# Kernel optimization log

Measured on AMD Instinct MI355X. Metric: run time of the kernel, lower is better.

Reference implementation:

```python
import jax, jax.numpy as jnp
import numpy as np

K_TOP = 2  # top-k experts per token


def setup_inputs() -> dict:
    key = jax.random.key(0)
    k1, k2, k3 = jax.random.split(key, 3)
    B, S, H, E = 4, 2048, 1024, 8
    hidden_states = jax.random.normal(k1, (B, S, H), dtype=jnp.float32)
    router_w = jax.random.normal(k2, (E, H), dtype=jnp.float32) * 0.02
    expert_weights = jax.random.normal(k3, (E, H, H), dtype=jnp.float32) * 0.02
    return {"hidden_states": hidden_states, "router_w": router_w, "expert_weights": expert_weights}


def reference(hidden_states, router_w, expert_weights):
    B, S, H = hidden_states.shape
    x = hidden_states.reshape(-1, H)                      # [N, H], N = B*S
    logits = x @ router_w.T                               # [N, E]
    probs = jax.nn.softmax(logits, axis=-1)               # [N, E]
    topk_vals, topk_idx = jax.lax.top_k(probs, K_TOP)     # [N, K]
    topk_w = topk_vals / (topk_vals.sum(-1, keepdims=True) + 1e-6)  # [N, K]

    # Dense per-expert GEMM over all tokens (single-device dispatch = identity)
    expert_out = jnp.einsum('nh,eho->eno', x, expert_weights)  # [E, N, H]

    # all_to_all_combine: gather each token's K expert outputs
    combined = jnp.take_along_axis(
        expert_out.transpose(1, 0, 2),                    # [N, E, H]
        topk_idx[:, :, None], axis=1)                     # [N, K, H]
    combined = combined.transpose(1, 0, 2)                # [K, N, H]

    # remap bias: sum over last dim of one-hot(topk_idx) * router_prob == gathered prob
    remap_bias = jnp.take_along_axis(probs, topk_idx, axis=1).T[:, :, None]  # [K, N, 1]

    weights = topk_w.T[:, :, None]                        # [K, N, 1]
    out = ((combined + remap_bias) * weights).sum(axis=0) # [N, H]
    return out.reshape(B, S, H)
```

## Files before the change

kernel.cpp:

```cpp
#include <hip/hip_runtime.h>
#include <hip/hip_fp16.h>
#include <cstdint>

typedef unsigned short u16;
typedef __attribute__((ext_vector_type(8))) short short8;
typedef __attribute__((ext_vector_type(4))) float float4v;

#define NTOK 8192
#define HDIM 1024
#define NEXP 8
#define TM 128
#define TN 128
#define BK 32
#define NITER (HDIM / BK)
#define ABUF (TM * BK)
#define MAXT 136
#define WBLK 8192
#define RBLK 2048

__device__ __forceinline__ u16 f2bf(float f) {
    union { float f; uint32_t u; } v; v.f = f;
    uint32_t u = v.u;
    return (u16)((u + 0x7FFFu + ((u >> 16) & 1u)) >> 16);
}

__device__ __forceinline__ void gll16(const u16* g, u16* l) {
    __builtin_amdgcn_global_load_lds(
        (const __attribute__((address_space(1))) uint32_t*)g,
        (__attribute__((address_space(3))) uint32_t*)l,
        16, 0, 0);
}

__global__ __launch_bounds__(256) void prep(const float* __restrict__ x,
                                            const float* __restrict__ rw,
                                            const float* __restrict__ ew,
                                            u16* __restrict__ x_bf,
                                            u16* __restrict__ w_bf,
                                            float* __restrict__ wt0,
                                            float* __restrict__ wt1,
                                            float* __restrict__ biasv,
                                            int* __restrict__ sel,
                                            int* __restrict__ ctrl) {
    if (blockIdx.x == 0 && threadIdx.x < 132) ctrl[threadIdx.x] = 0;

    if (blockIdx.x < WBLK) {
        __shared__ float tile[32][33];
        const int bid = blockIdx.x;
        const int e  = bid >> 10;
        const int k0 = (bid & 31) * 32;
        const int n0 = ((bid >> 5) & 31) * 32;
        const int r = threadIdx.x >> 3;
        const int c = (threadIdx.x & 7) * 4;
        const float4 v = *(const float4*)(ew + ((size_t)e << 20) + (size_t)(k0 + r) * HDIM + n0 + c);
        tile[r][c] = v.x; tile[r][c+1] = v.y; tile[r][c+2] = v.z; tile[r][c+3] = v.w;
        __syncthreads();
        ushort4 o;
        o.x = f2bf(tile[c][r]); o.y = f2bf(tile[c+1][r]);
        o.z = f2bf(tile[c+2][r]); o.w = f2bf(tile[c+3][r]);
        *(ushort4*)(w_bf + ((size_t)e << 20) + (size_t)(n0 + r) * HDIM + k0 + c) = o;
    } else {
        const int wv = threadIdx.x >> 6;
        const int l  = threadIdx.x & 63;
        const int n  = (blockIdx.x - WBLK) * 4 + wv;
        const float4* xr = (const float4*)(x + (size_t)n * HDIM);
        ushort4* xo = (ushort4*)(x_bf + (size_t)n * HDIM);

        float4 xv[4];
#pragma unroll
        for (int t = 0; t < 4; t++) {
            xv[t] = xr[t * 64 + l];
            ushort4 p;
            p.x = f2bf(xv[t].x); p.y = f2bf(xv[t].y);
            p.z = f2bf(xv[t].z); p.w = f2bf(xv[t].w);
            xo[t * 64 + l] = p;
        }

        float logits[NEXP];
#pragma unroll
        for (int e = 0; e < NEXP; e++) {
            const float4* rwe = (const float4*)(rw + e * HDIM);
            float acc = 0.f;
#pragma unroll
            for (int t = 0; t < 4; t++) {
                const float4 r = rwe[t * 64 + l];
                acc += xv[t].x * r.x + xv[t].y * r.y + xv[t].z * r.z + xv[t].w * r.w;
            }
#pragma unroll
            for (int s = 32; s > 0; s >>= 1) acc += __shfl_xor(acc, s, 64);
            logits[e] = acc;
        }

        if (l == 0) {
            float mx = logits[0];
#pragma unroll
            for (int e = 1; e < NEXP; e++) mx = fmaxf(mx, logits[e]);
            float p[NEXP]; float sum = 0.f;
#pragma unroll
            for (int e = 0; e < NEXP; e++) { p[e] = expf(logits[e] - mx); sum += p[e]; }
            const float inv = 1.f / sum;
#pragma unroll
            for (int e = 0; e < NEXP; e++) p[e] *= inv;
            int e0 = 0;
#pragma unroll
            for (int e = 1; e < NEXP; e++) if (p[e] > p[e0]) e0 = e;
            int e1 = (e0 == 0) ? 1 : 0;
#pragma unroll
            for (int e = 0; e < NEXP; e++) if (e != e0 && p[e] > p[e1]) e1 = e;
            const float p0 = p[e0], p1 = p[e1];
            const float wsum = p0 + p1 + 1e-6f;
            const float w0 = p0 / wsum, w1 = p1 / wsum;
            wt0[n] = w0; wt1[n] = w1;
            biasv[n] = w0 * p0 + w1 * p1;
            sel[n] = e0 | (e1 << 8);
        }
    }
}

__global__ __launch_bounds__(256) void build_lists(const int* __restrict__ sel,
                                                   int* __restrict__ lists,
                                                   int* __restrict__ ctrl,
                                                   int* __restrict__ tmap) {
    const int n  = blockIdx.x * 256 + threadIdx.x;
    const int wv = threadIdx.x >> 6;
    const int l  = threadIdx.x & 63;
    const int s  = sel[n];
    const int e0 = s & 0xFF, e1 = s >> 8;
    __shared__ int wcnt[NEXP][4];
    __shared__ int ebase[NEXP];
    int pf0 = 0, pf1 = 0;
    const unsigned long long ltmask = (1ULL << l) - 1ULL;
#pragma unroll
    for (int e = 0; e < NEXP; e++) {
        const int slot = (e0 == e) ? 0 : ((e1 == e) ? 1 : -1);
        const unsigned long long bal = __ballot(slot >= 0);
        const int pf = __popcll(bal & ltmask);
        if (slot == 0) pf0 = pf;
        if (slot == 1) pf1 = pf;
        if (l == 0) wcnt[e][wv] = __popcll(bal);
    }
    __syncthreads();
    if (threadIdx.x < NEXP) {
        const int e = threadIdx.x;
        const int tot = wcnt[e][0] + wcnt[e][1] + wcnt[e][2] + wcnt[e][3];
        ebase[e] = atomicAdd(&ctrl[e * 16], tot);
    }
    __syncthreads();
    int off0 = ebase[e0], off1 = ebase[e1];
#pragma unroll
    for (int i = 0; i < 4; i++) {
        off0 += (i < wv) ? wcnt[e0][i] : 0;
        off1 += (i < wv) ? wcnt[e1][i] : 0;
    }
    lists[e0 * NTOK + off0 + pf0] = n;
    lists[e1 * NTOK + off1 + pf1] = n | 0x10000;

    __shared__ int lastflag;
    __threadfence();
    if (threadIdx.x == 0) lastflag = (atomicAdd(&ctrl[128], 1) == (int)gridDim.x - 1);
    __syncthreads();
    if (lastflag) {
        __shared__ int tbase[NEXP + 1];
        if (threadIdx.x == 0) {
            int acc = 0;
            for (int e = 0; e < NEXP; e++) {
                tbase[e] = acc;
                acc += (atomicAdd(&ctrl[e * 16], 0) + TM - 1) / TM;
            }
            tbase[NEXP] = acc;
        }
        __syncthreads();
        for (int i = threadIdx.x; i < MAXT; i += 256) {
            int v = -1;
#pragma unroll
            for (int e = 0; e < NEXP; e++)
                if (i >= tbase[e] && i < tbase[e + 1]) v = (e << 16) | (i - tbase[e]);
            tmap[i] = v;
        }
    }
}

__global__ __launch_bounds__(256) void moe_gemm(const u16* __restrict__ x_bf,
                                                const u16* __restrict__ wt_bf,
                                                const int* __restrict__ lists,
                                                const int* __restrict__ ctrl,
                                                const int* __restrict__ tmap,
                                                const float* __restrict__ wt0,
                                                const float* __restrict__ wt1,
                                                const float* __restrict__ biasv,
                                                __half* __restrict__ stage0,
                                                __half* __restrict__ stage1) {
    const int ent = tmap[blockIdx.x];
    if (ent < 0) return;
    const int e = ent >> 16;
    const int tile_m = (ent & 0xFFFF) * TM;
    const int cnt = ctrl[e * 16];
    const int tn = blockIdx.y * TN;

    __shared__ u16 lA[3 * ABUF];
    __shared__ u16 lB[3 * ABUF];
    __shared__ int   toks[TM];
    __shared__ float wgt[TM];
    __shared__ float bia[TM];
    __shared__ int   slt[TM];

    const int t  = threadIdx.x;
    const int wv = t >> 6;
    const int l  = t & 63;

    if (t < TM) {
        const int idx = tile_m + t;
        int tok = 0; float w = 0.f, b = 0.f; int sl = 0;
        if (idx < cnt) {
            const int entry = lists[e * NTOK + idx];
            tok = entry & 0xFFFF;
            sl = entry >> 16;
            w = sl ? wt1[tok] : wt0[tok];
            b = sl ? 0.f : biasv[tok];
        }
        toks[t] = tok; wgt[t] = w; bia[t] = b; slt[t] = sl;
    }
    __syncthreads();

    const int r_in = l >> 2;
    const int koff = ((l & 3) ^ (r_in & 3)) * 8;
    const u16* pA[2]; const u16* pB[2]; int qoff[2];
#pragma unroll
    for (int i = 0; i < 2; i++) {
        const int c = wv * 2 + i;
        const int row = c * 16 + r_in;
        pA[i] = x_bf + (size_t)toks[row] * HDIM + koff;
        pB[i] = wt_bf + ((size_t)e << 20) + (size_t)(tn + row) * HDIM + koff;
        qoff[i] = c * 512;
    }

    const int wm = (wv & 1) * 64;
    const int wn = (wv >> 1) * 64;
    const int fm = l & 15;
    const int fq = l >> 4;
    int aoff[4], boff[4];
#pragma unroll
    for (int i = 0; i < 4; i++) {
        const int ra = wm + i * 16 + fm;
        const int rb = wn + i * 16 + fm;
        aoff[i] = ra * 32 + ((fq ^ (ra & 3)) * 8);
        boff[i] = rb * 32 + ((fq ^ (rb & 3)) * 8);
    }

    float4v acc[4][4];
#pragma unroll
    for (int i = 0; i < 4; i++)
#pragma unroll
        for (int j = 0; j < 4; j++) { float4v z = {0.f, 0.f, 0.f, 0.f}; acc[i][j] = z; }

    gll16(pA[0], lA + qoff[0]);
    gll16(pA[1], lA + qoff[1]);
    gll16(pB[0], lB + qoff[0]);
    gll16(pB[1], lB + qoff[1]);

    int cur = 0, nxt = 1;
    for (int it = 0; it < NITER; ++it) {
        if (it < NITER - 1) {
            const int nk = (it + 1) * BK;
            u16* la = lA + nxt * ABUF;
            u16* lb = lB + nxt * ABUF;
            gll16(pA[0] + nk, la + qoff[0]);
            gll16(pA[1] + nk, la + qoff[1]);
            gll16(pB[0] + nk, lb + qoff[0]);
            gll16(pB[1] + nk, lb + qoff[1]);
            asm volatile("s_waitcnt vmcnt(4)\n\ts_barrier" ::: "memory");
        } else {
            asm volatile("s_waitcnt vmcnt(0)\n\ts_barrier" ::: "memory");
        }

        const u16* ca = lA + cur * ABUF;
        const u16* cb = lB + cur * ABUF;
        short8 af[4], bf[4];
#pragma unroll
        for (int mf = 0; mf < 4; mf++) af[mf] = *(const short8*)&ca[aoff[mf]];
#pragma unroll
        for (int nf = 0; nf < 4; nf++) bf[nf] = *(const short8*)&cb[boff[nf]];
#pragma unroll
        for (int mf = 0; mf < 4; mf++)
#pragma unroll
            for (int nf = 0; nf < 4; nf++)
                acc[mf][nf] = __builtin_amdgcn_mfma_f32_16x16x32_bf16(af[mf], bf[nf], acc[mf][nf], 0, 0, 0);

        cur = nxt;
        nxt = (nxt == 2) ? 0 : nxt + 1;
    }

#pragma unroll
    for (int mf = 0; mf < 4; mf++) {
#pragma unroll
        for (int r = 0; r < 4; r++) {
            const int m_local = wm + mf * 16 + fq * 4 + r;
            if (tile_m + m_local < cnt) {
                const int tok = toks[m_local];
                const float w = wgt[m_local], b = bia[m_local];
                __half* sp = (slt[m_local] ? stage1 : stage0) + (size_t)tok * HDIM;
#pragma unroll
                for (int nf = 0; nf < 4; nf++) {
                    const int h = tn + wn + nf * 16 + fm;
                    sp[h] = __float2half(acc[mf][nf][r] * w + b);
                }
            }
        }
    }
}

__global__ __launch_bounds__(256) void combine(const __half* __restrict__ s0,
                                               const __half* __restrict__ s1,
                                               float* __restrict__ out) {
    const size_t idx = ((size_t)blockIdx.x * 256 + threadIdx.x) * 8;
    union { uint4 v; __half h[8]; } a, b;
    a.v = *(const uint4*)(s0 + idx);
    b.v = *(const uint4*)(s1 + idx);
    float4 o0, o1;
    o0.x = __half2float(a.h[0]) + __half2float(b.h[0]);
    o0.y = __half2float(a.h[1]) + __half2float(b.h[1]);
    o0.z = __half2float(a.h[2]) + __half2float(b.h[2]);
    o0.w = __half2float(a.h[3]) + __half2float(b.h[3]);
    o1.x = __half2float(a.h[4]) + __half2float(b.h[4]);
    o1.y = __half2float(a.h[5]) + __half2float(b.h[5]);
    o1.z = __half2float(a.h[6]) + __half2float(b.h[6]);
    o1.w = __half2float(a.h[7]) + __half2float(b.h[7]);
    *(float4*)(out + idx)     = o0;
    *(float4*)(out + idx + 4) = o1;
}

extern "C" void kernel_launch(void* const* d_in, const int* in_sizes, int n_in,
                              void* d_out, int out_size, void* d_ws, size_t ws_size,
                              hipStream_t stream) {
    const float* x  = (const float*)d_in[0];
    const float* rw = (const float*)d_in[1];
    const float* ew = (const float*)d_in[2];
    float* out = (float*)d_out;

    char* ws = (char*)d_ws;
    u16*    x_bf   = (u16*)ws;
    u16*    w_bf   = (u16*)(ws + 16777216);
    __half* stage0 = (__half*)(ws + 33554432);
    __half* stage1 = (__half*)(ws + 50331648);
    float*  wt0    = (float*)(ws + 67108864);
    float*  wt1    = (float*)(ws + 67141632);
    float*  biasv  = (float*)(ws + 67174400);
    int*    sel    = (int*)(ws + 67207168);
    int*    lists  = (int*)(ws + 67239936);
    int*    ctrl   = (int*)(ws + 67502080);
    int*    tmap   = (int*)(ws + 67502720);

    prep<<<WBLK + RBLK, 256, 0, stream>>>(x, rw, ew, x_bf, w_bf, wt0, wt1, biasv, sel, ctrl);
    build_lists<<<NTOK / 256, 256, 0, stream>>>(sel, lists, ctrl, tmap);
    moe_gemm<<<dim3(MAXT, HDIM / TN, 1), 256, 0, stream>>>(
        x_bf, w_bf, lists, ctrl, tmap, wt0, wt1, biasv, stage0, stage1);
    combine<<<(NTOK * HDIM) / (256 * 8), 256, 0, stream>>>(stage0, stage1, out);
}
```

Before: 201.9 us.

## Widen MoE GEMM tile to 128x256 with double-buffered LDS and new swizzle

Doubles the N tile so each block computes 128x256, with each wave owning a 64-column strip across all 128 rows (8x4 MFMA fragments per wave). This raises operand reuse per byte loaded from global memory. The LDS pipeline drops from triple to double buffering with a full wait at the top of each iteration, and the swizzle changes to XOR on (row>>1)&3. It also adds s_setprio around the MFMA bursts and caps occupancy at 2 blocks. In exchange it doubles the accumulator registers, halves the grid size in N, and may expose load latency because prefetch now overlaps less with compute.

```diff
diff --git a/kernel.cpp b/kernel.cpp
--- a/kernel.cpp
+++ b/kernel.cpp
@@ -10,10 +10,11 @@
 #define HDIM 1024
 #define NEXP 8
 #define TM 128
-#define TN 128
+#define TN 256
 #define BK 32
 #define NITER (HDIM / BK)
-#define ABUF (TM * BK)
+#define LA_N (TM * BK)
+#define LB_N (TN * BK)
 #define MAXT 136
 #define WBLK 8192
 #define RBLK 2048
@@ -179,16 +180,16 @@
     }
 }
 
-__global__ __launch_bounds__(256) void moe_gemm(const u16* __restrict__ x_bf,
-                                                const u16* __restrict__ wt_bf,
-                                                const int* __restrict__ lists,
-                                                const int* __restrict__ ctrl,
-                                                const int* __restrict__ tmap,
-                                                const float* __restrict__ wt0,
-                                                const float* __restrict__ wt1,
-                                                const float* __restrict__ biasv,
-                                                __half* __restrict__ stage0,
-                                                __half* __restrict__ stage1) {
+__global__ __launch_bounds__(256, 2) void moe_gemm(const u16* __restrict__ x_bf,
+                                                   const u16* __restrict__ wt_bf,
+                                                   const int* __restrict__ lists,
+                                                   const int* __restrict__ ctrl,
+                                                   const int* __restrict__ tmap,
+                                                   const float* __restrict__ wt0,
+                                                   const float* __restrict__ wt1,
+                                                   const float* __restrict__ biasv,
+                                                   __half* __restrict__ stage0,
+                                                   __half* __restrict__ stage1) {
     const int ent = tmap[blockIdx.x];
     if (ent < 0) return;
     const int e = ent >> 16;
@@ -196,8 +197,8 @@
     const int cnt = ctrl[e * 16];
     const int tn = blockIdx.y * TN;
 
-    __shared__ u16 lA[3 * ABUF];
-    __shared__ u16 lB[3 * ABUF];
+    __shared__ u16 lA[2 * LA_N];
+    __shared__ u16 lB[2 * LB_N];
     __shared__ int   toks[TM];
     __shared__ float wgt[TM];
     __shared__ float bia[TM];
@@ -221,86 +222,94 @@
     }
     __syncthreads();
 
-    const int r_in = l >> 2;
-    const int koff = ((l & 3) ^ (r_in & 3)) * 8;
-    const u16* pA[2]; const u16* pB[2]; int qoff[2];
+    const u16* gA[2]; int dA[2];
 #pragma unroll
     for (int i = 0; i < 2; i++) {
-        const int c = wv * 2 + i;
-        const int row = c * 16 + r_in;
-        pA[i] = x_bf + (size_t)toks[row] * HDIM + koff;
-        pB[i] = wt_bf + ((size_t)e << 20) + (size_t)(tn + row) * HDIM + koff;
-        qoff[i] = c * 512;
-    }
-
-    const int wm = (wv & 1) * 64;
-    const int wn = (wv >> 1) * 64;
+        const int slot = (i * 4 + wv) * 64 + l;
+        const int row  = slot >> 2;
+        const int c    = (slot & 3) ^ ((row >> 1) & 3);
+        gA[i] = x_bf + (size_t)toks[row] * HDIM + c * 8;
+        dA[i] = (i * 4 + wv) * 512;
+    }
+    const u16* gB[4]; int dB[4];
+#pragma unroll
+    for (int i = 0; i < 4; i++) {
+        const int slot = (i * 4 + wv) * 64 + l;
+        const int row  = slot >> 2;
+        const int c    = (slot & 3) ^ ((row >> 1) & 3);
+        gB[i] = wt_bf + ((size_t)e << 20) + (size_t)(tn + row) * HDIM + c * 8;
+        dB[i] = (i * 4 + wv) * 512;
+    }
+
     const int fm = l & 15;
     const int fq = l >> 4;
-    int aoff[4], boff[4];
-#pragma unroll
-    for (int i = 0; i < 4; i++) {
-        const int ra = wm + i * 16 + fm;
-        const int rb = wn + i * 16 + fm;
-        aoff[i] = ra * 32 + ((fq ^ (ra & 3)) * 8);
-        boff[i] = rb * 32 + ((fq ^ (rb & 3)) * 8);
-    }
-
-    float4v acc[4][4];
-#pragma unroll
-    for (int i = 0; i < 4; i++)
+    int aoff[8], boff[4];
+#pragma unroll
+    for (int mf = 0; mf < 8; mf++) {
+        const int r = mf * 16 + fm;
+        aoff[mf] = r * BK + ((fq ^ ((r >> 1) & 3)) * 8);
+    }
+#pragma unroll
+    for (int nf = 0; nf < 4; nf++) {
+        const int r = wv * 64 + nf * 16 + fm;
+        boff[nf] = r * BK + ((fq ^ ((r >> 1) & 3)) * 8);
+    }
+
+    float4v acc[8][4];
+#pragma unroll
+    for (int i = 0; i < 8; i++)
 #pragma unroll
         for (int j = 0; j < 4; j++) { float4v z = {0.f, 0.f, 0.f, 0.f}; acc[i][j] = z; }
 
-    gll16(pA[0], lA + qoff[0]);
-    gll16(pA[1], lA + qoff[1]);
-    gll16(pB[0], lB + qoff[0]);
-    gll16(pB[1], lB + qoff[1]);
-
-    int cur = 0, nxt = 1;
+#pragma unroll
+    for (int i = 0; i < 2; i++) gll16(gA[i], lA + dA[i]);
+#pragma unroll
+    for (int i = 0; i < 4; i++) gll16(gB[i], lB + dB[i]);
+
     for (int it = 0; it < NITER; ++it) {
-        if (it < NITER - 1) {
+        asm volatile("s_waitcnt vmcnt(0) lgkmcnt(0)\n\ts_barrier" ::: "memory");
+        if (it + 1 < NITER) {
             const int nk = (it + 1) * BK;
-            u16* la = lA + nxt * ABUF;
-            u16* lb = lB + nxt * ABUF;
-            gll16(pA[0] + nk, la + qoff[0]);
-            gll16(pA[1] + nk, la + qoff[1]);
-            gll16(pB[0] + nk, lb + qoff[0]);
-            gll16(pB[1] + nk, lb + qoff[1]);
-            asm volatile("s_waitcnt vmcnt(4)\n\ts_barrier" ::: "memory");
-        } else {
-            asm volatile("s_waitcnt vmcnt(0)\n\ts_barrier" ::: "memory");
-        }
-
-        const u16* ca = lA + cur * ABUF;
-        const u16* cb = lB + cur * ABUF;
-        short8 af[4], bf[4];
-#pragma unroll
-        for (int mf = 0; mf < 4; mf++) af[mf] = *(const short8*)&ca[aoff[mf]];
-#pragma unroll
-        for (int nf = 0; nf < 4; nf++) bf[nf] = *(const short8*)&cb[boff[nf]];
-#pragma unroll
-        for (int mf = 0; mf < 4; mf++)
-#pragma unroll
-            for (int nf = 0; nf < 4; nf++)
-                acc[mf][nf] = __builtin_amdgcn_mfma_f32_16x16x32_bf16(af[mf], bf[nf], acc[mf][nf], 0, 0, 0);
-
-        cur = nxt;
-        nxt = (nxt == 2) ? 0 : nxt + 1;
-    }
-
-#pragma unroll
-    for (int mf = 0; mf < 4; mf++) {
+            u16* la = lA + ((it + 1) & 1) * LA_N;
+            u16* lb = lB + ((it + 1) & 1) * LB_N;
+#pragma unroll
+            for (int i = 0; i < 2; i++) gll16(gA[i] + nk, la + dA[i]);
+#pragma unroll
+            for (int i = 0; i < 4; i++) gll16(gB[i] + nk, lb + dB[i]);
+        }
+        const u16* ca = lA + (it & 1) * LA_N;
+        const u16* cb = lB + (it & 1) * LB_N;
+        short8 bfr[4];
+#pragma unroll
+        for (int nf = 0; nf < 4; nf++) bfr[nf] = *(const short8*)&cb[boff[nf]];
+#pragma unroll
+        for (int mh = 0; mh < 2; mh++) {
+            short8 afr[4];
+#pragma unroll
+            for (int i = 0; i < 4; i++) afr[i] = *(const short8*)&ca[aoff[mh * 4 + i]];
+            __builtin_amdgcn_s_setprio(1);
+#pragma unroll
+            for (int i = 0; i < 4; i++)
+#pragma unroll
+                for (int nf = 0; nf < 4; nf++)
+                    acc[mh * 4 + i][nf] = __builtin_amdgcn_mfma_f32_16x16x32_bf16(
+                        afr[i], bfr[nf], acc[mh * 4 + i][nf], 0, 0, 0);
+            __builtin_amdgcn_s_setprio(0);
+        }
+    }
+
+#pragma unroll
+    for (int mf = 0; mf < 8; mf++) {
 #pragma unroll
         for (int r = 0; r < 4; r++) {
-            const int m_local = wm + mf * 16 + fq * 4 + r;
+            const int m_local = mf * 16 + fq * 4 + r;
             if (tile_m + m_local < cnt) {
                 const int tok = toks[m_local];
                 const float w = wgt[m_local], b = bia[m_local];
                 __half* sp = (slt[m_local] ? stage1 : stage0) + (size_t)tok * HDIM;
 #pragma unroll
                 for (int nf = 0; nf < 4; nf++) {
-                    const int h = tn + wn + nf * 16 + fm;
+                    const int h = tn + wv * 64 + nf * 16 + fm;
                     sp[h] = __float2half(acc[mf][nf][r] * w + b);
                 }
             }
```

New measurement: 207.2 us. +2.6%, slower.

## Deepen GEMM pipeline with register double-buffered fragments and priority hints

Applied to the files above, without the earlier changes.

Restructures the MoE GEMM main loop to prefetch three K-slices up front, keep two slices of global-to-LDS loads in flight, and double-buffer the MFMA operand fragments in registers so the next slice's LDS reads overlap the current MFMAs. It also changes the LDS swizzle to XOR on row>>1, remaps which thread loads which 16-byte chunk, fully unrolls the loop, raises wave priority around the MFMA block, and sets a minimum occupancy of 3 blocks via launch bounds. The goal is to hide LDS and global latency behind matrix math. In exchange it uses more registers, and the hand-written waitcnt counts must match the actual number of loads in flight or the loop reads stale data.

```diff
diff --git a/kernel.cpp b/kernel.cpp
--- a/kernel.cpp
+++ b/kernel.cpp
@@ -13,7 +13,8 @@
 #define TN 128
 #define BK 32
 #define NITER (HDIM / BK)
-#define ABUF (TM * BK)
+#define LA_N (TM * BK)
+#define LB_N (TN * BK)
 #define MAXT 136
 #define WBLK 8192
 #define RBLK 2048
@@ -179,16 +180,16 @@
     }
 }
 
-__global__ __launch_bounds__(256) void moe_gemm(const u16* __restrict__ x_bf,
-                                                const u16* __restrict__ wt_bf,
-                                                const int* __restrict__ lists,
-                                                const int* __restrict__ ctrl,
-                                                const int* __restrict__ tmap,
-                                                const float* __restrict__ wt0,
-                                                const float* __restrict__ wt1,
-                                                const float* __restrict__ biasv,
-                                                __half* __restrict__ stage0,
-                                                __half* __restrict__ stage1) {
+__global__ __launch_bounds__(256, 3) void moe_gemm(const u16* __restrict__ x_bf,
+                                                   const u16* __restrict__ wt_bf,
+                                                   const int* __restrict__ lists,
+                                                   const int* __restrict__ ctrl,
+                                                   const int* __restrict__ tmap,
+                                                   const float* __restrict__ wt0,
+                                                   const float* __restrict__ wt1,
+                                                   const float* __restrict__ biasv,
+                                                   __half* __restrict__ stage0,
+                                                   __half* __restrict__ stage1) {
     const int ent = tmap[blockIdx.x];
     if (ent < 0) return;
     const int e = ent >> 16;
@@ -196,8 +197,8 @@
     const int cnt = ctrl[e * 16];
     const int tn = blockIdx.y * TN;
 
-    __shared__ u16 lA[3 * ABUF];
-    __shared__ u16 lB[3 * ABUF];
+    __shared__ u16 lA[3 * LA_N];
+    __shared__ u16 lB[3 * LB_N];
     __shared__ int   toks[TM];
     __shared__ float wgt[TM];
     __shared__ float bia[TM];
@@ -221,16 +222,15 @@
     }
     __syncthreads();
 
-    const int r_in = l >> 2;
-    const int koff = ((l & 3) ^ (r_in & 3)) * 8;
-    const u16* pA[2]; const u16* pB[2]; int qoff[2];
+    const u16* gA[2]; const u16* gB[2]; int dAB[2];
 #pragma unroll
     for (int i = 0; i < 2; i++) {
-        const int c = wv * 2 + i;
-        const int row = c * 16 + r_in;
-        pA[i] = x_bf + (size_t)toks[row] * HDIM + koff;
-        pB[i] = wt_bf + ((size_t)e << 20) + (size_t)(tn + row) * HDIM + koff;
-        qoff[i] = c * 512;
+        const int slot = (i * 4 + wv) * 64 + l;
+        const int row  = slot >> 2;
+        const int c    = (slot & 3) ^ ((row >> 1) & 3);
+        gA[i] = x_bf + (size_t)toks[row] * HDIM + c * 8;
+        gB[i] = wt_bf + ((size_t)e << 20) + (size_t)(tn + row) * HDIM + c * 8;
+        dAB[i] = (i * 4 + wv) * 512;
     }
 
     const int wm = (wv & 1) * 64;
@@ -242,8 +242,8 @@
     for (int i = 0; i < 4; i++) {
         const int ra = wm + i * 16 + fm;
         const int rb = wn + i * 16 + fm;
-        aoff[i] = ra * 32 + ((fq ^ (ra & 3)) * 8);
-        boff[i] = rb * 32 + ((fq ^ (rb & 3)) * 8);
+        aoff[i] = ra * BK + ((fq ^ ((ra >> 1) & 3)) * 8);
+        boff[i] = rb * BK + ((fq ^ ((rb >> 1) & 3)) * 8);
     }
 
     float4v acc[4][4];
@@ -252,41 +252,66 @@
 #pragma unroll
         for (int j = 0; j < 4; j++) { float4v z = {0.f, 0.f, 0.f, 0.f}; acc[i][j] = z; }
 
-    gll16(pA[0], lA + qoff[0]);
-    gll16(pA[1], lA + qoff[1]);
-    gll16(pB[0], lB + qoff[0]);
-    gll16(pB[1], lB + qoff[1]);
-
-    int cur = 0, nxt = 1;
+    short8 afr[2][4], bfr[2][4];
+
+#pragma unroll
+    for (int tk = 0; tk < 3; tk++) {
+#pragma unroll
+        for (int i = 0; i < 2; i++) {
+            gll16(gA[i] + tk * BK, lA + tk * LA_N + dAB[i]);
+            gll16(gB[i] + tk * BK, lB + tk * LB_N + dAB[i]);
+        }
+    }
+    asm volatile("s_waitcnt vmcnt(8)\n\ts_barrier" ::: "memory");
+#pragma unroll
+    for (int i = 0; i < 4; i++) {
+        afr[0][i] = *(const short8*)&lA[aoff[i]];
+        bfr[0][i] = *(const short8*)&lB[boff[i]];
+    }
+
+#pragma unroll
     for (int it = 0; it < NITER; ++it) {
-        if (it < NITER - 1) {
-            const int nk = (it + 1) * BK;
-            u16* la = lA + nxt * ABUF;
-            u16* lb = lB + nxt * ABUF;
-            gll16(pA[0] + nk, la + qoff[0]);
-            gll16(pA[1] + nk, la + qoff[1]);
-            gll16(pB[0] + nk, lb + qoff[0]);
-            gll16(pB[1] + nk, lb + qoff[1]);
+        const int cs = it & 1;
+        const int ns = cs ^ 1;
+
+        if (it == 0) {
             asm volatile("s_waitcnt vmcnt(4)\n\ts_barrier" ::: "memory");
+        } else if (it < NITER - 1) {
+            asm volatile("s_waitcnt vmcnt(0)\n\ts_barrier" ::: "memory");
+        }
+
+        if (it >= 1 && it + 2 < NITER) {
+            const int nb = (it + 2) % 3;
+            const int nk = (it + 2) * BK;
+#pragma unroll
+            for (int i = 0; i < 2; i++) {
+                gll16(gA[i] + nk, lA + nb * LA_N + dAB[i]);
+                gll16(gB[i] + nk, lB + nb * LB_N + dAB[i]);
+            }
+        }
+
+        if (it + 1 < NITER) {
+            const u16* ca = lA + ((it + 1) % 3) * LA_N;
+            const u16* cb = lB + ((it + 1) % 3) * LB_N;
+#pragma unroll
+            for (int i = 0; i < 4; i++) {
+                afr[ns][i] = *(const short8*)&ca[aoff[i]];
+                bfr[ns][i] = *(const short8*)&cb[boff[i]];
+            }
+            asm volatile("s_waitcnt lgkmcnt(8)" ::: "memory");
         } else {
-            asm volatile("s_waitcnt vmcnt(0)\n\ts_barrier" ::: "memory");
-        }
-
-        const u16* ca = lA + cur * ABUF;
-        const u16* cb = lB + cur * ABUF;
-        short8 af[4], bf[4];
-#pragma unroll
-        for (int mf = 0; mf < 4; mf++) af[mf] = *(const short8*)&ca[aoff[mf]];
-#pragma unroll
-        for (int nf = 0; nf < 4; nf++) bf[nf] = *(const short8*)&cb[boff[nf]];
-#pragma unroll
-        for (int mf = 0; mf < 4; mf++)
+            asm volatile("s_waitcnt lgkmcnt(0)" ::: "memory");
+        }
+        __builtin_amdgcn_sched_barrier(0);
+
+        __builtin_amdgcn_s_setprio(1);
+#pragma unroll
+        for (int i = 0; i < 4; i++)
 #pragma unroll
             for (int nf = 0; nf < 4; nf++)
-                acc[mf][nf] = __builtin_amdgcn_mfma_f32_16x16x32_bf16(af[mf], bf[nf], acc[mf][nf], 0, 0, 0);
-
-        cur = nxt;
-        nxt = (nxt == 2) ? 0 : nxt + 1;
+                acc[i][nf] = __builtin_amdgcn_mfma_f32_16x16x32_bf16(
+                    afr[cs][i], bfr[cs][nf], acc[i][nf], 0, 0, 0);
+        __builtin_amdgcn_s_setprio(0);
     }
 
 #pragma unroll
```

New measurement: 196.1 us. 2.9% less time.
